# Optimization experiments

Hardware: AMD Instinct MI355X
Metric: run time of the kernel (lower is better)

## Reference

```python
import jax, jax.numpy as jnp
import numpy as np

S, D, A, H, C = 2048, 256, 64, 8, 64  # seq_len, node_dim, num_aux, num_heads, num_channels
QUAT = 4
N_TYPES = 3  # nodes, aux, rot


def _linear_params(key, out_dim, in_dim, use_bias=True):
    kw, kb = jax.random.split(key)
    lim = 1.0 / np.sqrt(in_dim)
    W = jax.random.uniform(kw, (out_dim, in_dim), minval=-lim, maxval=lim, dtype=jnp.float32)
    if not use_bias:
        return W, None
    b = jax.random.uniform(kb, (out_dim,), minval=-lim, maxval=lim, dtype=jnp.float32)
    return W, b


def setup_inputs() -> dict:
    key = jax.random.key(0)
    ks = jax.random.split(key, 8)
    nodes = jax.random.normal(ks[0], (S, D), dtype=jnp.float32)
    aux = jax.random.normal(ks[1], (S, A), dtype=jnp.float32)
    rot = jax.random.normal(ks[2], (S, QUAT), dtype=jnp.float32)
    W_nodes, b_nodes = _linear_params(ks[3], H * C * 2, D)
    W_aux, b_aux = _linear_params(ks[4], H * C * 2, A)
    W_rot, _ = _linear_params(ks[5], H * C * 2, QUAT, use_bias=False)
    W_val, b_val = _linear_params(ks[6], D * H * N_TYPES, D)
    return {
        "nodes": nodes, "aux": aux, "rot": rot,
        "W_nodes": W_nodes, "b_nodes": b_nodes,
        "W_aux": W_aux, "b_aux": b_aux,
        "W_rot": W_rot,
        "W_val": W_val, "b_val": b_val,
    }


def reference(nodes, aux, rot, W_nodes, b_nodes, W_aux, b_aux, W_rot, W_val, b_val):
    seq_len = nodes.shape[0]
    # values: (S, 3H, D)
    val = (nodes @ W_val.T + b_val).reshape(seq_len, N_TYPES * H, -1)
    # per-source k/q: each (S, H, C)
    nodes_k, nodes_q = jnp.split((nodes @ W_nodes.T + b_nodes).reshape(seq_len, H, -1), 2, -1)
    aux_k, aux_q = jnp.split((aux @ W_aux.T + b_aux).reshape(seq_len, H, -1), 2, -1)
    rot_k, rot_q = jnp.split((rot @ W_rot.T).reshape(seq_len, H, -1), 2, -1)
    # concat along head axis -> (S, 3H, C)
    k = jnp.concatenate([nodes_k, aux_k, rot_k], axis=-2)
    q = jnp.concatenate([nodes_q, aux_q, rot_q], axis=-2)
    # (S, S, 3H) score tensor, scaled by 1/sqrt(num_heads) as in the original
    logits = jnp.einsum('ihc,jhc->ijh', k, q) / jnp.sqrt(jnp.asarray(H, nodes.dtype))
    att = jax.nn.softmax(logits, axis=-2)  # softmax over the j (key) axis
    out = jnp.einsum('ijh,jhd->id', att, val)  # (S, D)
    return out
```

## Files before the change

### kernel.cpp

```cpp
#include <hip/hip_runtime.h>

#define S_LEN 2048
#define NHEAD 24
#define CDIM 64
#define DDIM 256

typedef _Float16 f16x8 __attribute__((ext_vector_type(8)));
typedef float f32x4 __attribute__((ext_vector_type(4)));

__device__ __forceinline__ ushort f2h(float f) {
    _Float16 h = (_Float16)f;
    return __builtin_bit_cast(ushort, h);
}
__device__ __forceinline__ uint pkh(float a, float b) {
    auto v = __builtin_amdgcn_cvt_pkrtz(a, b);
    return __builtin_bit_cast(uint, v);
}

__device__ __forceinline__ int4 cvt8(const float* __restrict__ p) {
    float4 a = *(const float4*)p;
    float4 b = *(const float4*)(p + 4);
    f16x8 h;
    h[0] = (_Float16)a.x; h[1] = (_Float16)a.y;
    h[2] = (_Float16)a.z; h[3] = (_Float16)a.w;
    h[4] = (_Float16)b.x; h[5] = (_Float16)b.y;
    h[6] = (_Float16)b.z; h[7] = (_Float16)b.w;
    return __builtin_bit_cast(int4, h);
}

__global__ __launch_bounds__(256) void gemm_bt_kernel(
    const float* __restrict__ A, const float* __restrict__ W,
    const float* __restrict__ bias, int M, int N, int K,
    int mode, int hbase,
    ushort* __restrict__ Kbuf, ushort* __restrict__ Qbuf, ushort* __restrict__ Vt)
{
    __shared__ ushort Asub[64 * 40];
    __shared__ ushort Wsub[64 * 40];
    const int tid = threadIdx.x;
    const int wave = tid >> 6, lane = tid & 63;
    const int g = lane >> 4, c = lane & 15;
    const int m0 = blockIdx.y * 64, n0 = blockIdx.x * 64;
    const int srow = tid >> 2;
    const int skk = (tid & 3) * 8;

    f32x4 acc[4] = {f32x4{0,0,0,0}, f32x4{0,0,0,0}, f32x4{0,0,0,0}, f32x4{0,0,0,0}};

    for (int k0 = 0; k0 < K; k0 += 32) {
        __syncthreads();
        *(int4*)&Asub[srow * 40 + skk] = cvt8(&A[(m0 + srow) * K + k0 + skk]);
        *(int4*)&Wsub[srow * 40 + skk] = cvt8(&W[(n0 + srow) * K + k0 + skk]);
        __syncthreads();
        f16x8 af = *(const f16x8*)&Asub[(wave * 16 + c) * 40 + g * 8];
#pragma unroll
        for (int t = 0; t < 4; t++) {
            f16x8 bf = *(const f16x8*)&Wsub[(t * 16 + c) * 40 + g * 8];
            acc[t] = __builtin_amdgcn_mfma_f32_16x16x32_f16(af, bf, acc[t], 0, 0, 0);
        }
    }

#pragma unroll
    for (int t = 0; t < 4; t++) {
        int n = n0 + t * 16 + c;
        float bv = bias[n];
#pragma unroll
        for (int r = 0; r < 4; r++) {
            int m = m0 + wave * 16 + g * 4 + r;
            ushort u = f2h(acc[t][r] + bv);
            if (mode == 0) {
                int h = hbase + (n >> 7);
                int cc = n & 127;
                if (cc < 64) Kbuf[(h * S_LEN + m) * CDIM + cc] = u;
                else         Qbuf[(h * S_LEN + m) * CDIM + cc - 64] = u;
            } else {
                int h = n >> 8;
                int d = n & 255;
                Vt[(h * DDIM + d) * S_LEN + m] = u;
            }
        }
    }
}

__global__ __launch_bounds__(256) void rot_proj_kernel(
    const float* __restrict__ rot, const float* __restrict__ Wrot,
    ushort* __restrict__ Kbuf, ushort* __restrict__ Qbuf)
{
    int idx = blockIdx.x * 256 + threadIdx.x;
    int i = idx >> 10, n = idx & 1023;
    float4 r = *(const float4*)&rot[i * 4];
    float4 w = *(const float4*)&Wrot[n * 4];
    float v = r.x * w.x + r.y * w.y + r.z * w.z + r.w * w.w;
    int h = 16 + (n >> 7), cc = n & 127;
    ushort u = f2h(v);
    if (cc < 64) Kbuf[(h * S_LEN + i) * CDIM + cc] = u;
    else         Qbuf[(h * S_LEN + i) * CDIM + cc - 64] = u;
}

__global__ __launch_bounds__(256) void zero_kernel(float* __restrict__ p) {
    p[blockIdx.x * 256 + threadIdx.x] = 0.f;
}

__global__ __launch_bounds__(256) void flash_kernel(
    const ushort* __restrict__ Kbuf, const ushort* __restrict__ Qbuf,
    const ushort* __restrict__ Vt, float* __restrict__ out)
{
    __shared__ ushort Qlds[2][64 * 72];
    __shared__ ushort Plds[2][64 * 72];
    __shared__ float  Alds[2][64];

    const int tid = threadIdx.x;
    const int wave = tid >> 6, lane = tid & 63;
    const int g = lane >> 4, c = lane & 15;
    const int h = blockIdx.y;
    const int i0 = blockIdx.x * 64;
    const float SC = 0.51006973f;

    const ushort* Krow = &Kbuf[(h * S_LEN + i0 + wave * 16 + c) * CDIM + g * 8];
    f16x8 ka0 = *(const f16x8*)Krow;
    f16x8 ka1 = *(const f16x8*)(Krow + 32);

    const ushort* Vbase = &Vt[(h * DDIM + wave * 64 + c) * S_LEN + g * 8];

    const int qi0 = tid, qi1 = tid + 256;
    const int qr0 = qi0 >> 3, qc0 = (qi0 & 7) * 8;
    const int qr1 = qi1 >> 3, qc1 = (qi1 & 7) * 8;

    *(int4*)&Qlds[0][qr0 * 72 + qc0] =
        *(const int4*)&Qbuf[(h * S_LEN + qr0) * CDIM + qc0];
    *(int4*)&Qlds[0][qr1 * 72 + qc1] =
        *(const int4*)&Qbuf[(h * S_LEN + qr1) * CDIM + qc1];
    __syncthreads();

    f32x4 acc[16];
#pragma unroll
    for (int t = 0; t < 16; t++) acc[t] = f32x4{0, 0, 0, 0};
    float mrow = -1e30f, lrow = 0.f;

    for (int j0 = 0; j0 < S_LEN; j0 += 64) {
        const int cur = (j0 >> 6) & 1, nxt = cur ^ 1;

        const int jn = j0 + 64;
        int4 qn0 = *(const int4*)&Qbuf[(h * S_LEN + jn + qr0) * CDIM + qc0];
        int4 qn1 = *(const int4*)&Qbuf[(h * S_LEN + jn + qr1) * CDIM + qc1];

        f16x8 vf0[4], vf1[4];
#pragma unroll
        for (int t = 0; t < 4; t++) {
            const ushort* Vr = Vbase + (t * 16) * S_LEN + j0;
            vf0[t] = *(const f16x8*)Vr;
            vf1[t] = *(const f16x8*)(Vr + 32);
        }

        f32x4 Sf[4];
#pragma unroll
        for (int jc = 0; jc < 4; jc++) {
            const ushort* Qr = &Qlds[cur][(jc * 16 + c) * 72 + g * 8];
            f16x8 qb0 = *(const f16x8*)Qr;
            f16x8 qb1 = *(const f16x8*)(Qr + 32);
            f32x4 s = {0, 0, 0, 0};
            s = __builtin_amdgcn_mfma_f32_16x16x32_f16(qb0, ka0, s, 0, 0, 0);
            s = __builtin_amdgcn_mfma_f32_16x16x32_f16(qb1, ka1, s, 0, 0, 0);
            Sf[jc] = s * SC;
        }

        float nm = -1e30f;
#pragma unroll
        for (int jc = 0; jc < 4; jc++)
            nm = fmaxf(nm, fmaxf(fmaxf(Sf[jc][0], Sf[jc][1]),
                                 fmaxf(Sf[jc][2], Sf[jc][3])));
        nm = fmaxf(nm, __shfl_xor(nm, 16));
        nm = fmaxf(nm, __shfl_xor(nm, 32));
        nm = fmaxf(nm, mrow);
        float alpha = exp2f(mrow - nm);

        float rs = 0.f;
#pragma unroll
        for (int jc = 0; jc < 4; jc++) {
            float p0 = exp2f(Sf[jc][0] - nm);
            float p1 = exp2f(Sf[jc][1] - nm);
            float p2 = exp2f(Sf[jc][2] - nm);
            float p3 = exp2f(Sf[jc][3] - nm);
            rs += (p0 + p1) + (p2 + p3);
            uint2 w;
            w.x = pkh(p0, p1);
            w.y = pkh(p2, p3);
            *(uint2*)&Plds[cur][(wave * 16 + c) * 72 + jc * 16 + g * 4] = w;
        }
        rs += __shfl_xor(rs, 16);
        rs += __shfl_xor(rs, 32);
        lrow = lrow * alpha + rs;
        mrow = nm;
        if (g == 0) Alds[cur][wave * 16 + c] = alpha;

        *(int4*)&Qlds[nxt][qr0 * 72 + qc0] = qn0;
        *(int4*)&Qlds[nxt][qr1 * 72 + qc1] = qn1;

        __syncthreads();

#pragma unroll
        for (int b = 0; b < 4; b++) {
            f32x4 ab = *(const f32x4*)&Alds[cur][b * 16 + g * 4];
#pragma unroll
            for (int t = 0; t < 4; t++) acc[b * 4 + t] *= ab;
        }

#pragma unroll
        for (int b = 0; b < 4; b++) {
            const ushort* Pr = &Plds[cur][(b * 16 + c) * 72 + g * 8];
            f16x8 pa0 = *(const f16x8*)Pr;
            f16x8 pa1 = *(const f16x8*)(Pr + 32);
#pragma unroll
            for (int t = 0; t < 4; t++) {
                acc[b * 4 + t] = __builtin_amdgcn_mfma_f32_16x16x32_f16(pa0, vf0[t], acc[b * 4 + t], 0, 0, 0);
                acc[b * 4 + t] = __builtin_amdgcn_mfma_f32_16x16x32_f16(pa1, vf1[t], acc[b * 4 + t], 0, 0, 0);
            }
        }
    }

    __syncthreads();
    if (g == 0) Alds[0][wave * 16 + c] = 1.0f / lrow;
    __syncthreads();
#pragma unroll
    for (int b = 0; b < 4; b++) {
        f32x4 lb = *(const f32x4*)&Alds[0][b * 16 + g * 4];
#pragma unroll
        for (int t = 0; t < 4; t++)
#pragma unroll
            for (int r = 0; r < 4; r++) {
                int i = i0 + b * 16 + g * 4 + r;
                int d = wave * 64 + t * 16 + c;
                atomicAdd(&out[i * DDIM + d], acc[b * 4 + t][r] * lb[r]);
            }
    }
}

extern "C" void kernel_launch(void* const* d_in, const int* in_sizes, int n_in,
                              void* d_out, int out_size, void* d_ws, size_t ws_size,
                              hipStream_t stream) {
    const float *nodes = 0, *aux = 0, *rot = 0, *W_nodes = 0, *b_nodes = 0,
                *W_aux = 0, *b_aux = 0, *W_rot = 0, *W_val = 0, *b_val = 0;
    int i1024[2] = {-1, -1};
    int n1024 = 0;
    for (int i = 0; i < n_in; ++i) {
        const float* p = (const float*)d_in[i];
        switch (in_sizes[i]) {
            case 524288:  nodes   = p; break;
            case 131072:  aux     = p; break;
            case 8192:    rot     = p; break;
            case 262144:  W_nodes = p; break;
            case 65536:   W_aux   = p; break;
            case 4096:    W_rot   = p; break;
            case 1572864: W_val   = p; break;
            case 6144:    b_val   = p; break;
            case 1024:    if (n1024 < 2) i1024[n1024] = i; n1024++; break;
            default: break;
        }
    }
    if (n1024 == 2) {
        b_nodes = (const float*)d_in[i1024[0]];
        b_aux   = (const float*)d_in[i1024[1]];
    }
    if (!nodes || !aux || !rot || !W_nodes || !b_nodes || !W_aux || !b_aux ||
        !W_rot || !W_val || !b_val) {
        nodes   = (const float*)d_in[0];
        aux     = (const float*)d_in[1];
        rot     = (const float*)d_in[2];
        W_nodes = (const float*)d_in[3];
        b_nodes = (const float*)d_in[4];
        W_aux   = (const float*)d_in[5];
        b_aux   = (const float*)d_in[6];
        W_rot   = (const float*)d_in[7];
        W_val   = (const float*)d_in[8];
        b_val   = (const float*)d_in[9];
    }
    float* out = (float*)d_out;

    float*  Opad = (float*)d_ws;
    ushort* Kbuf = (ushort*)(Opad + S_LEN * DDIM);
    ushort* Qbuf = Kbuf + NHEAD * S_LEN * CDIM;
    ushort* Vt   = Qbuf + NHEAD * S_LEN * CDIM;

    dim3 blk(256);
    zero_kernel<<<dim3(S_LEN * DDIM / 256), blk, 0, stream>>>(out);
    gemm_bt_kernel<<<dim3(16, 32), blk, 0, stream>>>(nodes, W_nodes, b_nodes,
        2048, 1024, 256, 0, 0, Kbuf, Qbuf, nullptr);
    gemm_bt_kernel<<<dim3(16, 32), blk, 0, stream>>>(aux, W_aux, b_aux,
        2048, 1024, 64, 0, 8, Kbuf, Qbuf, nullptr);
    rot_proj_kernel<<<dim3(8192), blk, 0, stream>>>(rot, W_rot, Kbuf, Qbuf);
    gemm_bt_kernel<<<dim3(96, 32), blk, 0, stream>>>(nodes, W_val, b_val,
        2048, 6144, 256, 1, 0, nullptr, nullptr, Vt);
    flash_kernel<<<dim3(32, NHEAD), blk, 0, stream>>>(Kbuf, Qbuf, Vt, out);
}
```

Before: 272.0 us.

## Use 128x128 fp16 GEMM with pre-converted inputs for value projection

Adds kernels that convert nodes and W_val to fp16 once, and a new 128x128-tile MFMA GEMM with K-step 64 for the value projection. The transposed Vt stores now write four packed fp16 values per store instead of single scattered halves. This cuts the repeated fp32-to-fp16 conversion, raises data reuse per block and improves store coalescing. In exchange it adds two conversion launches and extra workspace traffic.

```diff
diff --git a/kernel.cpp b/kernel.cpp
--- a/kernel.cpp
+++ b/kernel.cpp
@@ -15,6 +15,9 @@
 __device__ __forceinline__ uint pkh(float a, float b) {
     auto v = __builtin_amdgcn_cvt_pkrtz(a, b);
     return __builtin_bit_cast(uint, v);
+}
+__device__ __forceinline__ uint pk2(float a, float b) {
+    return (uint)f2h(a) | ((uint)f2h(b) << 16);
 }
 
 __device__ __forceinline__ int4 cvt8(const float* __restrict__ p) {
@@ -28,11 +31,82 @@
     return __builtin_bit_cast(int4, h);
 }
 
+__global__ __launch_bounds__(256) void cvt16_kernel(
+    const float* __restrict__ src, ushort* __restrict__ dst, int n8)
+{
+    int idx = blockIdx.x * 256 + threadIdx.x;
+    if (idx < n8) *(int4*)&dst[idx * 8] = cvt8(&src[idx * 8]);
+}
+
+__global__ __launch_bounds__(256) void gemm128_kernel(
+    const ushort* __restrict__ A16, const ushort* __restrict__ W16,
+    const float* __restrict__ bias, int K, ushort* __restrict__ Vt)
+{
+    __shared__ ushort Asub[128 * 72];
+    __shared__ ushort Wsub[128 * 72];
+    const int tid = threadIdx.x;
+    const int wave = tid >> 6, lane = tid & 63;
+    const int g = lane >> 4, c = lane & 15;
+    const int wm = wave & 1, wn = wave >> 1;
+    const int m0 = blockIdx.y * 128, n0 = blockIdx.x * 128;
+
+    f32x4 acc[16];
+#pragma unroll
+    for (int t = 0; t < 16; t++) acc[t] = f32x4{0, 0, 0, 0};
+
+    for (int k0 = 0; k0 < K; k0 += 64) {
+        __syncthreads();
+#pragma unroll
+        for (int q = 0; q < 4; q++) {
+            int i = tid + 256 * q;
+            int row = i >> 3, kc = (i & 7) * 8;
+            *(int4*)&Asub[row * 72 + kc] = *(const int4*)&A16[(m0 + row) * K + k0 + kc];
+            *(int4*)&Wsub[row * 72 + kc] = *(const int4*)&W16[(n0 + row) * K + k0 + kc];
+        }
+        __syncthreads();
+
+        f16x8 af0[4], af1[4];
+#pragma unroll
+        for (int mt = 0; mt < 4; mt++) {
+            const ushort* Ar = &Asub[(wm * 64 + mt * 16 + c) * 72 + g * 8];
+            af0[mt] = *(const f16x8*)Ar;
+            af1[mt] = *(const f16x8*)(Ar + 32);
+        }
+#pragma unroll
+        for (int nt = 0; nt < 4; nt++) {
+            const ushort* Wr = &Wsub[(wn * 64 + nt * 16 + c) * 72 + g * 8];
+            f16x8 bf0 = *(const f16x8*)Wr;
+            f16x8 bf1 = *(const f16x8*)(Wr + 32);
+#pragma unroll
+            for (int mt = 0; mt < 4; mt++) {
+                acc[mt * 4 + nt] = __builtin_amdgcn_mfma_f32_16x16x32_f16(af0[mt], bf0, acc[mt * 4 + nt], 0, 0, 0);
+                acc[mt * 4 + nt] = __builtin_amdgcn_mfma_f32_16x16x32_f16(af1[mt], bf1, acc[mt * 4 + nt], 0, 0, 0);
+            }
+        }
+    }
+
+#pragma unroll
+    for (int nt = 0; nt < 4; nt++) {
+        int n = n0 + wn * 64 + nt * 16 + c;
+        float bv = bias[n];
+        int h = n >> 8, d = n & 255;
+#pragma unroll
+        for (int mt = 0; mt < 4; mt++) {
+            int m = m0 + wm * 64 + mt * 16 + g * 4;
+            f32x4 v = acc[mt * 4 + nt];
+            uint2 pw;
+            pw.x = pk2(v[0] + bv, v[1] + bv);
+            pw.y = pk2(v[2] + bv, v[3] + bv);
+            *(uint2*)&Vt[(h * DDIM + d) * S_LEN + m] = pw;
+        }
+    }
+}
+
 __global__ __launch_bounds__(256) void gemm_bt_kernel(
     const float* __restrict__ A, const float* __restrict__ W,
     const float* __restrict__ bias, int M, int N, int K,
-    int mode, int hbase,
-    ushort* __restrict__ Kbuf, ushort* __restrict__ Qbuf, ushort* __restrict__ Vt)
+    int hbase,
+    ushort* __restrict__ Kbuf, ushort* __restrict__ Qbuf)
 {
     __shared__ ushort Asub[64 * 40];
     __shared__ ushort Wsub[64 * 40];
@@ -66,16 +140,10 @@
         for (int r = 0; r < 4; r++) {
             int m = m0 + wave * 16 + g * 4 + r;
             ushort u = f2h(acc[t][r] + bv);
-            if (mode == 0) {
-                int h = hbase + (n >> 7);
-                int cc = n & 127;
-                if (cc < 64) Kbuf[(h * S_LEN + m) * CDIM + cc] = u;
-                else         Qbuf[(h * S_LEN + m) * CDIM + cc - 64] = u;
-            } else {
-                int h = n >> 8;
-                int d = n & 255;
-                Vt[(h * DDIM + d) * S_LEN + m] = u;
-            }
+            int h = hbase + (n >> 7);
+            int cc = n & 127;
+            if (cc < 64) Kbuf[(h * S_LEN + m) * CDIM + cc] = u;
+            else         Qbuf[(h * S_LEN + m) * CDIM + cc - 64] = u;
         }
     }
 }
@@ -278,15 +346,19 @@
     ushort* Kbuf = (ushort*)(Opad + S_LEN * DDIM);
     ushort* Qbuf = Kbuf + NHEAD * S_LEN * CDIM;
     ushort* Vt   = Qbuf + NHEAD * S_LEN * CDIM;
+    ushort* nodes16 = Vt + NHEAD * DDIM * S_LEN;
+    ushort* Wval16  = nodes16 + 524288;
 
     dim3 blk(256);
     zero_kernel<<<dim3(S_LEN * DDIM / 256), blk, 0, stream>>>(out);
+    cvt16_kernel<<<dim3(256), blk, 0, stream>>>(nodes, nodes16, 524288 / 8);
+    cvt16_kernel<<<dim3(768), blk, 0, stream>>>(W_val, Wval16, 1572864 / 8);
     gemm_bt_kernel<<<dim3(16, 32), blk, 0, stream>>>(nodes, W_nodes, b_nodes,
-        2048, 1024, 256, 0, 0, Kbuf, Qbuf, nullptr);
+        2048, 1024, 256, 0, Kbuf, Qbuf);
     gemm_bt_kernel<<<dim3(16, 32), blk, 0, stream>>>(aux, W_aux, b_aux,
-        2048, 1024, 64, 0, 8, Kbuf, Qbuf, nullptr);
+        2048, 1024, 64, 8, Kbuf, Qbuf);
     rot_proj_kernel<<<dim3(8192), blk, 0, stream>>>(rot, W_rot, Kbuf, Qbuf);
-    gemm_bt_kernel<<<dim3(96, 32), blk, 0, stream>>>(nodes, W_val, b_val,
-        2048, 6144, 256, 1, 0, nullptr, nullptr, Vt);
+    gemm128_kernel<<<dim3(48, 16), blk, 0, stream>>>(nodes16, Wval16, b_val,
+        256, Vt);
     flash_kernel<<<dim3(32, NHEAD), blk, 0, stream>>>(Kbuf, Qbuf, Vt, out);
 }
```

Result: faster. 256.5 us (-5.7%).
